# Optimization experiments

Hardware: AMD Instinct MI355X
Metric: run time of the kernel (lower is better)

## Reference

```python
import jax, jax.numpy as jnp
import numpy as np

WIN = 7  # window size (w1 = w2 = 7)

def _rel_pos_indices(w: int) -> jnp.ndarray:
    # Matches RelPosBias 2-D branch: [(w*w), (w*w)] indices into (2w-1)^2 table
    p = np.arange(w)
    gi, gj = np.meshgrid(p, p, indexing='ij')
    grid = np.stack([gi.reshape(-1), gj.reshape(-1)], axis=-1)  # [w*w, 2]
    rel = grid[:, None, :] - grid[None, :, :]                   # [w*w, w*w, 2]
    rel = rel + (w - 1)
    idx = rel[..., 0] * (2 * w - 1) + rel[..., 1]               # [w*w, w*w]
    return jnp.asarray(idx, dtype=jnp.int32)


def setup_inputs() -> dict:
    key = jax.random.key(0)
    k1, k2, k3, k4 = jax.random.split(key, 4)
    dim, heads = 256, 8
    b, gx, gy = 64, 8, 8
    x = jax.random.normal(k1, (b, gx, gy, WIN, WIN, dim), dtype=jnp.float32)
    # torch nn.Linear weight layout: [out_features, in_features]
    w_qkv = jax.random.normal(k2, (3 * dim, dim), dtype=jnp.float32) * (dim ** -0.5)
    w_out = jax.random.normal(k3, (dim, dim), dtype=jnp.float32) * (dim ** -0.5)
    rel_emb = jax.random.normal(k4, ((2 * WIN - 1) ** 2, heads), dtype=jnp.float32) * 0.02
    rel_idx = _rel_pos_indices(WIN)
    return {"x": x, "w_qkv": w_qkv, "w_out": w_out, "rel_emb": rel_emb, "rel_idx": rel_idx}


def reference(x, w_qkv, w_out, rel_emb, rel_idx):
    b, gx, gy, w1, w2, d = x.shape
    h = rel_emb.shape[1]          # heads
    dh = d // h                    # dim_head
    scale = dh ** -0.5
    n = w1 * w2                    # tokens per window (49)

    xr = x.reshape(b * gx * gy, n, d)                        # (B, n, d)
    qkv = jnp.einsum('bnd,ed->bne', xr, w_qkv)               # (B, n, 3d)
    q, k, v = jnp.split(qkv, 3, axis=-1)
    split_heads = lambda t: t.reshape(t.shape[0], n, h, dh).transpose(0, 2, 1, 3)
    q, k, v = map(split_heads, (q, k, v))                    # (B, h, n, dh)

    sim = jnp.einsum('bhid,bhjd->bhij', q * scale, k)        # (B, h, n, n)
    bias = rel_emb[rel_idx]                                   # (n, n, h)
    sim = sim + bias.transpose(2, 0, 1)[None]                 # + (1, h, n, n)
    attn = jax.nn.softmax(sim, axis=-1)

    out = jnp.einsum('bhij,bhjd->bhid', attn, v)              # (B, h, n, dh)
    out = out.transpose(0, 2, 1, 3).reshape(-1, w1, w2, d)    # (B, w1, w2, d)
    out = jnp.einsum('bxyd,ed->bxye', out, w_out)
    return out.reshape(b, gx, gy, w1, w2, d)
```

## Files before the change

### kernel.cpp

```cpp
#include <hip/hip_runtime.h>
#include <hip/hip_bf16.h>

typedef __bf16 bf16x8 __attribute__((ext_vector_type(8)));
typedef __bf16 bf16x4v __attribute__((ext_vector_type(4)));
typedef float f32x4 __attribute__((ext_vector_type(4)));

#define MFMA(a, b, c) __builtin_amdgcn_mfma_f32_16x16x32_bf16((a), (b), (c), 0, 0, 0)

#define NEG_BIG (-1e30f)

#define XO_LD 264
#define W_LD 136
#define QK_LD 40
#define VT_LD 72
#define P_LD 72

__global__ __launch_bounds__(256) void prep_kernel(
    const float* __restrict__ w_qkv, const float* __restrict__ w_out,
    const float* __restrict__ rel_emb, const int* __restrict__ rel_idx,
    __bf16* __restrict__ wqkv_b, __bf16* __restrict__ wout_b,
    float* __restrict__ bias) {
  const float kScale = 0.17677669529663687f;
  int idx = blockIdx.x * 256 + threadIdx.x;
  if (idx < 196608) {
    float v = w_qkv[idx];
    if (idx < 65536) v *= kScale;
    wqkv_b[idx] = (__bf16)v;
  } else if (idx < 262144) {
    int j = idx - 196608;
    wout_b[j] = (__bf16)w_out[j];
  } else if (idx < 294912) {
    int j = idx - 262144;
    int h = j >> 12, i = (j >> 6) & 63, c = j & 63;
    float v = NEG_BIG;
    if (i < 49 && c < 49) v = rel_emb[rel_idx[i * 49 + c] * 8 + h];
    bias[j] = v;
  }
}

__global__ __launch_bounds__(256, 2) void attn_kernel(
    const float* __restrict__ x, const __bf16* __restrict__ wqkv,
    const __bf16* __restrict__ wout, const float* __restrict__ bias,
    float* __restrict__ out) {
  __shared__ __attribute__((aligned(16))) __bf16 s_xo[64 * XO_LD];
  __shared__ __attribute__((aligned(16))) __bf16 s_r2[96 * W_LD];

  __bf16* q_s = s_r2;
  __bf16* k_s = s_r2 + 2560;
  __bf16* vt_s = s_r2 + 5120;
  __bf16* p_s = s_r2 + 7424;

  const int tid = threadIdx.x;
  const int wave = tid >> 6;
  const int lane = tid & 63;
  const int quad = lane >> 4;
  const int l16 = lane & 15;
  const int i0 = wave * 16 + quad * 4;
  const int am = wave * 16 + l16;

  const f32x4 fzero = {0.f, 0.f, 0.f, 0.f};

  {
    const float4* xg = (const float4*)(x + (size_t)blockIdx.x * 12544);
    for (int i = tid; i < 3136; i += 256) {
      float4 v = xg[i];
      int row = i >> 6, c4 = (i & 63) << 2;
      bf16x4v t;
      t[0] = (__bf16)v.x; t[1] = (__bf16)v.y; t[2] = (__bf16)v.z; t[3] = (__bf16)v.w;
      *(bf16x4v*)&s_xo[row * XO_LD + c4] = t;
    }
    bf16x4v z;
    z[0] = z[1] = z[2] = z[3] = (__bf16)0.0f;
    for (int i = tid; i < 960; i += 256) {
      int row = 49 + (i >> 6), c4 = (i & 63) << 2;
      *(bf16x4v*)&s_xo[row * XO_LD + c4] = z;
    }
  }
  __syncthreads();

  bf16x8 afr[8];
  {
    const __bf16* base = &s_xo[am * XO_LD + quad * 8];
#pragma unroll
    for (int kk = 0; kk < 8; ++kk) afr[kk] = *(const bf16x8*)(base + kk * 32);
  }

  for (int h = 0; h < 8; ++h) {
    f32x4 acc[6];
#pragma unroll
    for (int t = 0; t < 6; ++t) acc[t] = fzero;

#pragma unroll
    for (int kh = 0; kh < 2; ++kh) {
      __syncthreads();
      for (int i = tid; i < 1536; i += 256) {
        int lr = i >> 4, c = (i & 15) * 8;
        int grow = (lr >> 5) * 256 + h * 32 + (lr & 31);
        *(bf16x8*)&s_r2[lr * W_LD + c] =
            *(const bf16x8*)&wqkv[grow * 256 + kh * 128 + c];
      }
      __syncthreads();
#pragma unroll
      for (int k2 = 0; k2 < 4; ++k2) {
        bf16x8 a = afr[kh * 4 + k2];
#pragma unroll
        for (int t = 0; t < 6; ++t) {
          bf16x8 b = *(const bf16x8*)&s_r2[(t * 16 + l16) * W_LD + k2 * 32 + quad * 8];
          acc[t] = MFMA(a, b, acc[t]);
        }
      }
    }
    __syncthreads();

#pragma unroll
    for (int t = 0; t < 2; ++t) {
#pragma unroll
      for (int r = 0; r < 4; ++r) {
        q_s[(i0 + r) * QK_LD + t * 16 + l16] = (__bf16)acc[t][r];
        k_s[(i0 + r) * QK_LD + t * 16 + l16] = (__bf16)acc[2 + t][r];
      }
      bf16x4v pv;
#pragma unroll
      for (int r = 0; r < 4; ++r) pv[r] = (__bf16)acc[4 + t][r];
      *(bf16x4v*)&vt_s[(t * 16 + l16) * VT_LD + i0] = pv;
    }
    __syncthreads();

    f32x4 s[4];
    {
      const float* bb = bias + (h << 12);
#pragma unroll
      for (int nt = 0; nt < 4; ++nt)
#pragma unroll
        for (int r = 0; r < 4; ++r) s[nt][r] = bb[(i0 + r) * 64 + nt * 16 + l16];
      bf16x8 a = *(const bf16x8*)&q_s[am * QK_LD + quad * 8];
#pragma unroll
      for (int nt = 0; nt < 4; ++nt) {
        bf16x8 b = *(const bf16x8*)&k_s[(nt * 16 + l16) * QK_LD + quad * 8];
        s[nt] = MFMA(a, b, s[nt]);
      }
    }

#pragma unroll
    for (int r = 0; r < 4; ++r) {
      float mx = fmaxf(fmaxf(s[0][r], s[1][r]), fmaxf(s[2][r], s[3][r]));
      mx = fmaxf(mx, __shfl_xor(mx, 1));
      mx = fmaxf(mx, __shfl_xor(mx, 2));
      mx = fmaxf(mx, __shfl_xor(mx, 4));
      mx = fmaxf(mx, __shfl_xor(mx, 8));
      float e0 = __expf(s[0][r] - mx), e1 = __expf(s[1][r] - mx);
      float e2 = __expf(s[2][r] - mx), e3 = __expf(s[3][r] - mx);
      float sm = e0 + e1 + e2 + e3;
      sm += __shfl_xor(sm, 1);
      sm += __shfl_xor(sm, 2);
      sm += __shfl_xor(sm, 4);
      sm += __shfl_xor(sm, 8);
      float rs = 1.0f / sm;
      int row = i0 + r;
      p_s[row * P_LD + l16] = (__bf16)(e0 * rs);
      p_s[row * P_LD + 16 + l16] = (__bf16)(e1 * rs);
      p_s[row * P_LD + 32 + l16] = (__bf16)(e2 * rs);
      p_s[row * P_LD + 48 + l16] = (__bf16)(e3 * rs);
    }
    __syncthreads();

    f32x4 oa[2];
    oa[0] = fzero;
    oa[1] = fzero;
#pragma unroll
    for (int kk = 0; kk < 2; ++kk) {
      bf16x8 a = *(const bf16x8*)&p_s[am * P_LD + kk * 32 + quad * 8];
#pragma unroll
      for (int t = 0; t < 2; ++t) {
        bf16x8 b = *(const bf16x8*)&vt_s[(t * 16 + l16) * VT_LD + kk * 32 + quad * 8];
        oa[t] = MFMA(a, b, oa[t]);
      }
    }
#pragma unroll
    for (int t = 0; t < 2; ++t)
#pragma unroll
      for (int r = 0; r < 4; ++r)
        s_xo[(i0 + r) * XO_LD + h * 32 + t * 16 + l16] = (__bf16)oa[t][r];
  }
  __syncthreads();

  for (int ec = 0; ec < 8; ++ec) {
    for (int i = tid; i < 1024; i += 256) {
      int lr = i >> 5, c = (i & 31) * 8;
      *(bf16x8*)&s_r2[lr * XO_LD + c] = *(const bf16x8*)&wout[(ec * 32 + lr) * 256 + c];
    }
    __syncthreads();
    f32x4 fa[2];
    fa[0] = fzero;
    fa[1] = fzero;
#pragma unroll
    for (int kk = 0; kk < 8; ++kk) {
      bf16x8 a = *(const bf16x8*)&s_xo[am * XO_LD + kk * 32 + quad * 8];
#pragma unroll
      for (int t = 0; t < 2; ++t) {
        bf16x8 b = *(const bf16x8*)&s_r2[(t * 16 + l16) * XO_LD + kk * 32 + quad * 8];
        fa[t] = MFMA(a, b, fa[t]);
      }
    }
    float* ob = out + (size_t)blockIdx.x * 12544 + ec * 32;
#pragma unroll
    for (int t = 0; t < 2; ++t)
#pragma unroll
      for (int r = 0; r < 4; ++r) {
        int row = i0 + r;
        if (row < 49) ob[row * 256 + t * 16 + l16] = fa[t][r];
      }
    __syncthreads();
  }
}

extern "C" void kernel_launch(void* const* d_in, const int* in_sizes, int n_in,
                              void* d_out, int out_size, void* d_ws, size_t ws_size,
                              hipStream_t stream) {
  (void)in_sizes; (void)n_in; (void)out_size; (void)ws_size;
  const float* x = (const float*)d_in[0];
  const float* w_qkv = (const float*)d_in[1];
  const float* w_out = (const float*)d_in[2];
  const float* rel_emb = (const float*)d_in[3];
  const int* rel_idx = (const int*)d_in[4];
  float* out = (float*)d_out;

  char* ws = (char*)d_ws;
  __bf16* wqkv_b = (__bf16*)ws;
  __bf16* wout_b = (__bf16*)(ws + 393216);
  float* bias = (float*)(ws + 524288);

  prep_kernel<<<1152, 256, 0, stream>>>(w_qkv, w_out, rel_emb, rel_idx,
                                        wqkv_b, wout_b, bias);
  attn_kernel<<<4096, 256, 0, stream>>>(x, wqkv_b, wout_b, bias, out);
}
```

Baseline: 864.2 us.

## Shrink shared memory to one buffer and keep attention output in registers

Shared memory becomes a single compact buffer: the x tile region is reused for weight staging, and Q/K/V^T/P get tighter row strides. Per-head attention outputs are held in registers (ofr) instead of being written back to the x tile, and launch bounds rise to 4 blocks per CU. The output projection stages 64 weight rows per sync instead of 32, halving its barrier count. The aim is higher occupancy and fewer syncs, at the cost of more register pressure and split 8-byte LDS loads on the odd strides.

```diff
diff --git a/kernel.cpp b/kernel.cpp
--- a/kernel.cpp
+++ b/kernel.cpp
@@ -6,14 +6,31 @@
 typedef float f32x4 __attribute__((ext_vector_type(4)));
 
 #define MFMA(a, b, c) __builtin_amdgcn_mfma_f32_16x16x32_bf16((a), (b), (c), 0, 0, 0)
-
 #define NEG_BIG (-1e30f)
 
 #define XO_LD 264
 #define W_LD 136
-#define QK_LD 40
+#define QK_LD 36
 #define VT_LD 72
-#define P_LD 72
+#define P_LD 68
+#define OTR_LD 36
+
+#define WR_ELS (96 * W_LD)
+#define P_OFF 0
+#define OTR_OFF (64 * P_LD)
+#define Q_OFF WR_ELS
+#define K_OFF (Q_OFF + 64 * QK_LD)
+#define VT_OFF (K_OFF + 64 * QK_LD)
+#define TOTAL_ELS (VT_OFF + 32 * VT_LD)
+
+static __device__ inline bf16x8 ld8x2(const __bf16* p) {
+  bf16x4v lo = *(const bf16x4v*)p;
+  bf16x4v hi = *(const bf16x4v*)(p + 4);
+  bf16x8 r;
+  r[0] = lo[0]; r[1] = lo[1]; r[2] = lo[2]; r[3] = lo[3];
+  r[4] = hi[0]; r[5] = hi[1]; r[6] = hi[2]; r[7] = hi[3];
+  return r;
+}
 
 __global__ __launch_bounds__(256) void prep_kernel(
     const float* __restrict__ w_qkv, const float* __restrict__ w_out,
@@ -38,17 +55,11 @@
   }
 }
 
-__global__ __launch_bounds__(256, 2) void attn_kernel(
+__global__ __launch_bounds__(256, 4) void attn_kernel(
     const float* __restrict__ x, const __bf16* __restrict__ wqkv,
     const __bf16* __restrict__ wout, const float* __restrict__ bias,
     float* __restrict__ out) {
-  __shared__ __attribute__((aligned(16))) __bf16 s_xo[64 * XO_LD];
-  __shared__ __attribute__((aligned(16))) __bf16 s_r2[96 * W_LD];
-
-  __bf16* q_s = s_r2;
-  __bf16* k_s = s_r2 + 2560;
-  __bf16* vt_s = s_r2 + 5120;
-  __bf16* p_s = s_r2 + 7424;
+  __shared__ __attribute__((aligned(16))) __bf16 sm[TOTAL_ELS];
 
   const int tid = threadIdx.x;
   const int wave = tid >> 6;
@@ -67,23 +78,23 @@
       int row = i >> 6, c4 = (i & 63) << 2;
       bf16x4v t;
       t[0] = (__bf16)v.x; t[1] = (__bf16)v.y; t[2] = (__bf16)v.z; t[3] = (__bf16)v.w;
-      *(bf16x4v*)&s_xo[row * XO_LD + c4] = t;
+      *(bf16x4v*)&sm[row * XO_LD + c4] = t;
     }
     bf16x4v z;
     z[0] = z[1] = z[2] = z[3] = (__bf16)0.0f;
     for (int i = tid; i < 960; i += 256) {
       int row = 49 + (i >> 6), c4 = (i & 63) << 2;
-      *(bf16x4v*)&s_xo[row * XO_LD + c4] = z;
+      *(bf16x4v*)&sm[row * XO_LD + c4] = z;
     }
   }
   __syncthreads();
 
   bf16x8 afr[8];
-  {
-    const __bf16* base = &s_xo[am * XO_LD + quad * 8];
-#pragma unroll
-    for (int kk = 0; kk < 8; ++kk) afr[kk] = *(const bf16x8*)(base + kk * 32);
-  }
+#pragma unroll
+  for (int kk = 0; kk < 8; ++kk)
+    afr[kk] = *(const bf16x8*)&sm[am * XO_LD + kk * 32 + quad * 8];
+
+  bf16x8 ofr[8];
 
   for (int h = 0; h < 8; ++h) {
     f32x4 acc[6];
@@ -96,7 +107,7 @@
       for (int i = tid; i < 1536; i += 256) {
         int lr = i >> 4, c = (i & 15) * 8;
         int grow = (lr >> 5) * 256 + h * 32 + (lr & 31);
-        *(bf16x8*)&s_r2[lr * W_LD + c] =
+        *(bf16x8*)&sm[lr * W_LD + c] =
             *(const bf16x8*)&wqkv[grow * 256 + kh * 128 + c];
       }
       __syncthreads();
@@ -105,62 +116,64 @@
         bf16x8 a = afr[kh * 4 + k2];
 #pragma unroll
         for (int t = 0; t < 6; ++t) {
-          bf16x8 b = *(const bf16x8*)&s_r2[(t * 16 + l16) * W_LD + k2 * 32 + quad * 8];
+          bf16x8 b = *(const bf16x8*)&sm[(t * 16 + l16) * W_LD + k2 * 32 + quad * 8];
           acc[t] = MFMA(a, b, acc[t]);
         }
       }
     }
-    __syncthreads();
-
-#pragma unroll
-    for (int t = 0; t < 2; ++t) {
-#pragma unroll
-      for (int r = 0; r < 4; ++r) {
-        q_s[(i0 + r) * QK_LD + t * 16 + l16] = (__bf16)acc[t][r];
-        k_s[(i0 + r) * QK_LD + t * 16 + l16] = (__bf16)acc[2 + t][r];
-      }
-      bf16x4v pv;
-#pragma unroll
-      for (int r = 0; r < 4; ++r) pv[r] = (__bf16)acc[4 + t][r];
-      *(bf16x4v*)&vt_s[(t * 16 + l16) * VT_LD + i0] = pv;
-    }
-    __syncthreads();
-
-    f32x4 s[4];
+
+    f32x4 sim[4];
     {
       const float* bb = bias + (h << 12);
 #pragma unroll
       for (int nt = 0; nt < 4; ++nt)
 #pragma unroll
-        for (int r = 0; r < 4; ++r) s[nt][r] = bb[(i0 + r) * 64 + nt * 16 + l16];
-      bf16x8 a = *(const bf16x8*)&q_s[am * QK_LD + quad * 8];
+        for (int r = 0; r < 4; ++r) sim[nt][r] = bb[(i0 + r) * 64 + nt * 16 + l16];
+    }
+
+#pragma unroll
+    for (int t = 0; t < 2; ++t) {
+#pragma unroll
+      for (int r = 0; r < 4; ++r) {
+        sm[Q_OFF + (i0 + r) * QK_LD + t * 16 + l16] = (__bf16)acc[t][r];
+        sm[K_OFF + (i0 + r) * QK_LD + t * 16 + l16] = (__bf16)acc[2 + t][r];
+      }
+      bf16x4v pv;
+#pragma unroll
+      for (int r = 0; r < 4; ++r) pv[r] = (__bf16)acc[4 + t][r];
+      *(bf16x4v*)&sm[VT_OFF + (t * 16 + l16) * VT_LD + i0] = pv;
+    }
+    __syncthreads();
+
+    {
+      bf16x8 a = ld8x2(&sm[Q_OFF + am * QK_LD + quad * 8]);
 #pragma unroll
       for (int nt = 0; nt < 4; ++nt) {
-        bf16x8 b = *(const bf16x8*)&k_s[(nt * 16 + l16) * QK_LD + quad * 8];
-        s[nt] = MFMA(a, b, s[nt]);
+        bf16x8 b = ld8x2(&sm[K_OFF + (nt * 16 + l16) * QK_LD + quad * 8]);
+        sim[nt] = MFMA(a, b, sim[nt]);
       }
     }
 
 #pragma unroll
     for (int r = 0; r < 4; ++r) {
-      float mx = fmaxf(fmaxf(s[0][r], s[1][r]), fmaxf(s[2][r], s[3][r]));
+      float mx = fmaxf(fmaxf(sim[0][r], sim[1][r]), fmaxf(sim[2][r], sim[3][r]));
       mx = fmaxf(mx, __shfl_xor(mx, 1));
       mx = fmaxf(mx, __shfl_xor(mx, 2));
       mx = fmaxf(mx, __shfl_xor(mx, 4));
       mx = fmaxf(mx, __shfl_xor(mx, 8));
-      float e0 = __expf(s[0][r] - mx), e1 = __expf(s[1][r] - mx);
-      float e2 = __expf(s[2][r] - mx), e3 = __expf(s[3][r] - mx);
-      float sm = e0 + e1 + e2 + e3;
-      sm += __shfl_xor(sm, 1);
-      sm += __shfl_xor(sm, 2);
-      sm += __shfl_xor(sm, 4);
-      sm += __shfl_xor(sm, 8);
-      float rs = 1.0f / sm;
+      float e0 = __expf(sim[0][r] - mx), e1 = __expf(sim[1][r] - mx);
+      float e2 = __expf(sim[2][r] - mx), e3 = __expf(sim[3][r] - mx);
+      float sum = e0 + e1 + e2 + e3;
+      sum += __shfl_xor(sum, 1);
+      sum += __shfl_xor(sum, 2);
+      sum += __shfl_xor(sum, 4);
+      sum += __shfl_xor(sum, 8);
+      float rs = 1.0f / sum;
       int row = i0 + r;
-      p_s[row * P_LD + l16] = (__bf16)(e0 * rs);
-      p_s[row * P_LD + 16 + l16] = (__bf16)(e1 * rs);
-      p_s[row * P_LD + 32 + l16] = (__bf16)(e2 * rs);
-      p_s[row * P_LD + 48 + l16] = (__bf16)(e3 * rs);
+      sm[P_OFF + row * P_LD + l16] = (__bf16)(e0 * rs);
+      sm[P_OFF + row * P_LD + 16 + l16] = (__bf16)(e1 * rs);
+      sm[P_OFF + row * P_LD + 32 + l16] = (__bf16)(e2 * rs);
+      sm[P_OFF + row * P_LD + 48 + l16] = (__bf16)(e3 * rs);
     }
     __syncthreads();
 
@@ -169,10 +182,10 @@
     oa[1] = fzero;
 #pragma unroll
     for (int kk = 0; kk < 2; ++kk) {
-      bf16x8 a = *(const bf16x8*)&p_s[am * P_LD + kk * 32 + quad * 8];
+      bf16x8 a = ld8x2(&sm[P_OFF + am * P_LD + kk * 32 + quad * 8]);
 #pragma unroll
       for (int t = 0; t < 2; ++t) {
-        bf16x8 b = *(const bf16x8*)&vt_s[(t * 16 + l16) * VT_LD + kk * 32 + quad * 8];
+        bf16x8 b = *(const bf16x8*)&sm[VT_OFF + (t * 16 + l16) * VT_LD + kk * 32 + quad * 8];
         oa[t] = MFMA(a, b, oa[t]);
       }
     }
@@ -180,37 +193,41 @@
     for (int t = 0; t < 2; ++t)
 #pragma unroll
       for (int r = 0; r < 4; ++r)
-        s_xo[(i0 + r) * XO_LD + h * 32 + t * 16 + l16] = (__bf16)oa[t][r];
-  }
-  __syncthreads();
-
-  for (int ec = 0; ec < 8; ++ec) {
-    for (int i = tid; i < 1024; i += 256) {
+        sm[OTR_OFF + (i0 + r) * OTR_LD + t * 16 + l16] = (__bf16)oa[t][r];
+    __syncthreads();
+    ofr[h] = ld8x2(&sm[OTR_OFF + am * OTR_LD + quad * 8]);
+  }
+
+  for (int rr = 0; rr < 4; ++rr) {
+    __syncthreads();
+    for (int i = tid; i < 2048; i += 256) {
       int lr = i >> 5, c = (i & 31) * 8;
-      *(bf16x8*)&s_r2[lr * XO_LD + c] = *(const bf16x8*)&wout[(ec * 32 + lr) * 256 + c];
-    }
-    __syncthreads();
-    f32x4 fa[2];
-    fa[0] = fzero;
-    fa[1] = fzero;
-#pragma unroll
-    for (int kk = 0; kk < 8; ++kk) {
-      bf16x8 a = *(const bf16x8*)&s_xo[am * XO_LD + kk * 32 + quad * 8];
-#pragma unroll
-      for (int t = 0; t < 2; ++t) {
-        bf16x8 b = *(const bf16x8*)&s_r2[(t * 16 + l16) * XO_LD + kk * 32 + quad * 8];
-        fa[t] = MFMA(a, b, fa[t]);
-      }
-    }
-    float* ob = out + (size_t)blockIdx.x * 12544 + ec * 32;
-#pragma unroll
-    for (int t = 0; t < 2; ++t)
-#pragma unroll
-      for (int r = 0; r < 4; ++r) {
-        int row = i0 + r;
-        if (row < 49) ob[row * 256 + t * 16 + l16] = fa[t][r];
-      }
-    __syncthreads();
+      *(bf16x8*)&sm[lr * XO_LD + c] = *(const bf16x8*)&wout[(rr * 64 + lr) * 256 + c];
+    }
+    __syncthreads();
+#pragma unroll
+    for (int e2 = 0; e2 < 2; ++e2) {
+      f32x4 fa[2];
+      fa[0] = fzero;
+      fa[1] = fzero;
+#pragma unroll
+      for (int kk = 0; kk < 8; ++kk) {
+        bf16x8 a = ofr[kk];
+#pragma unroll
+        for (int t = 0; t < 2; ++t) {
+          bf16x8 b = *(const bf16x8*)&sm[(e2 * 32 + t * 16 + l16) * XO_LD + kk * 32 + quad * 8];
+          fa[t] = MFMA(a, b, fa[t]);
+        }
+      }
+      float* ob = out + (size_t)blockIdx.x * 12544 + (rr * 2 + e2) * 32;
+#pragma unroll
+      for (int t = 0; t < 2; ++t)
+#pragma unroll
+        for (int r = 0; r < 4; ++r) {
+          int row = i0 + r;
+          if (row < 49) ob[row * 256 + t * 16 + l16] = fa[t][r];
+        }
+    }
   }
 }
 
```

Result: faster. 844.6 us (-2.3%).
